# Optimization experiments

Measured on AMD Instinct MI355X. Metric: run time of the kernel, lower is better.

Reference implementation:

```python
import jax, jax.numpy as jnp
import numpy as np

N, D, K = 100000, 512, 1024

def setup_inputs() -> dict:
    key = jax.random.key(0)
    k1, k2 = jax.random.split(key)
    nodes = jax.random.normal(k1, (N, D), dtype=jnp.float32)
    # Faithful to original: indices sampled in [0, d) (torch.randint(d, ...))
    center_ind = jax.random.randint(k2, (K,), 0, D, dtype=jnp.int32)
    return {"nodes": nodes, "center_ind": center_ind, "num_clusters": K}


def reference(nodes, center_ind, num_clusters):
    # nodes: [n, d]; initial centers gathered from nodes (indices in [0, d) per original code)
    centers0 = nodes[center_ind]                      # [K, d]
    # Squared L2 distances via the expansion trick; avoids materializing [K, n, d].
    # argmin over squared distance == argmin over distance (sqrt is monotone).
    node_sq = jnp.sum(nodes * nodes, axis=1)          # [n]
    cent_sq = jnp.sum(centers0 * centers0, axis=1)    # [K]
    # d2[k, i] = ||c_k||^2 + ||x_i||^2 - 2 c_k . x_i
    d2 = cent_sq[:, None] + node_sq[None, :] - 2.0 * jnp.einsum("kd,nd->kn", centers0, nodes)
    assignment = jnp.argmin(d2, axis=0)               # [n]
    # Scatter-add nodes into their assigned cluster (index_add equivalent).
    centers = jax.ops.segment_sum(nodes, assignment, num_segments=num_clusters)  # [K, d]
    return centers
```

## Files before the change

### kernel.cpp

```cpp
#include <hip/hip_runtime.h>
#include <stdint.h>


typedef _Float16 f16x8  __attribute__((ext_vector_type(8)));
typedef float    f32x4  __attribute__((ext_vector_type(4)));

#define DD 512
#define KK 1024

static __device__ __forceinline__ unsigned orderable(float s) {
    unsigned u = __float_as_uint(s);
    return (u & 0x80000000u) ? ~u : (u | 0x80000000u);
}

__global__ void canon_first(const int* __restrict__ center_ind,
                            unsigned* __restrict__ firstk, int K) {
    int k = (int)(blockIdx.x * blockDim.x + threadIdx.x);
    if (k < K) atomicMin(&firstk[center_ind[k]], (unsigned)k);
}
__global__ void canon_map(const int* __restrict__ center_ind,
                          const unsigned* __restrict__ firstk,
                          unsigned* __restrict__ canon, int K) {
    int k = (int)(blockIdx.x * blockDim.x + threadIdx.x);
    if (k < K) canon[k] = firstk[center_ind[k]];
}

__global__ void gather_centers(const float* __restrict__ nodes,
                               const int* __restrict__ center_ind,
                               _Float16* __restrict__ centf,
                               float* __restrict__ cent_sq,
                               int K) {
    int k    = (int)blockIdx.x;
    int lane = (int)threadIdx.x;
    int ci   = center_ind[k];
    const f32x4* p = reinterpret_cast<const f32x4*>(nodes + (size_t)ci * DD + lane * 8);
    f32x4 v0 = p[0], v1 = p[1];
    f16x8 h;
    h[0]=(_Float16)v0[0]; h[1]=(_Float16)v0[1]; h[2]=(_Float16)v0[2]; h[3]=(_Float16)v0[3];
    h[4]=(_Float16)v1[0]; h[5]=(_Float16)v1[1]; h[6]=(_Float16)v1[2]; h[7]=(_Float16)v1[3];
    int t = k >> 4, r = k & 15;
    *reinterpret_cast<f16x8*>(centf + ((size_t)((t * 64 + lane) * 16 + r) << 3)) = h;
    float ssq = v0[0]*v0[0]+v0[1]*v0[1]+v0[2]*v0[2]+v0[3]*v0[3]
              + v1[0]*v1[0]+v1[1]*v1[1]+v1[2]*v1[2]+v1[3]*v1[3];
    #pragma unroll
    for (int off = 32; off > 0; off >>= 1) ssq += __shfl_xor(ssq, off, 64);
    if (lane == 0) cent_sq[k] = ssq;
}

__launch_bounds__(512, 4)
__global__ void assign_mfma(const float* __restrict__ nodes,
                            const _Float16* __restrict__ centf,
                            const float* __restrict__ cent_sq,
                            const unsigned* __restrict__ canon,
                            unsigned* __restrict__ assignment,
                            unsigned* __restrict__ counts,
                            int N, int K) {
    __shared__ __align__(16) _Float16 nt[64 * DD];
    __shared__ float csq[KK];
    __shared__ unsigned long long best[64];

    const int tid = (int)threadIdx.x;
    const int n0  = (int)blockIdx.x * 64;

    #pragma unroll
    for (int it = 0; it < 8; ++it) {
        int f   = it * 512 + tid;
        int row = f >> 6;
        int d0  = (f & 63) << 3;
        f32x4 v0 = {0.f,0.f,0.f,0.f}, v1 = {0.f,0.f,0.f,0.f};
        if (n0 + row < N) {
            const f32x4* p = reinterpret_cast<const f32x4*>(nodes + (size_t)(n0 + row) * DD + d0);
            v0 = p[0]; v1 = p[1];
        }
        f16x8 h;
        h[0]=(_Float16)v0[0]; h[1]=(_Float16)v0[1]; h[2]=(_Float16)v0[2]; h[3]=(_Float16)v0[3];
        h[4]=(_Float16)v1[0]; h[5]=(_Float16)v1[1]; h[6]=(_Float16)v1[2]; h[7]=(_Float16)v1[3];
        int byte = ((row << 10) + (d0 << 1)) ^ ((row & 7) << 4);
        *reinterpret_cast<f16x8*>(reinterpret_cast<char*>(nt) + byte) = h;
    }
    for (int j = tid; j < K;  j += 512) csq[j]  = cent_sq[j];
    for (int j = tid; j < 64; j += 512) best[j] = ~0ULL;
    __syncthreads();

    const int lane = tid & 63;
    const int wid  = tid >> 6;
    const int l15  = lane & 15;
    const int g    = lane >> 4;
    const int swz  = (l15 & 7) << 4;
    char* ntb = reinterpret_cast<char*>(nt);
    const int cw0 = wid * (K >> 3);

    int bbase[4];
    #pragma unroll
    for (int nG = 0; nG < 4; ++nG) bbase[nG] = (((nG * 16 + l15) << 10) + (g << 4));

    #define LA(dst, tg_, s_)                                                         \
        { _Pragma("unroll")                                                          \
          for (int t_ = 0; t_ < 2; ++t_)                                             \
              dst[t_] = *reinterpret_cast<const f16x8*>(                             \
                  centf + ((size_t)((cw0 >> 4) + (tg_) * 2 + t_) << 13)              \
                        + ((s_) << 9) + (lane << 3)); }
    #define LB(dst, s_)                                                              \
        { _Pragma("unroll")                                                          \
          for (int nG = 0; nG < 4; ++nG)                                             \
              dst[nG] = *reinterpret_cast<const f16x8*>(                             \
                  ntb + ((bbase[nG] + ((s_) << 6)) ^ swz)); }
    #define MM(Av, Bv)                                                               \
        { _Pragma("unroll")                                                          \
          for (int t_ = 0; t_ < 2; ++t_)                                             \
              _Pragma("unroll")                                                      \
              for (int nG = 0; nG < 4; ++nG)                                         \
                  acc[t_][nG] = __builtin_amdgcn_mfma_f32_16x16x32_f16(              \
                      Av[t_], Bv[nG], acc[t_][nG], 0, 0, 0); }

    f16x8 Av[2];
    f16x8 Bv[4];

    #pragma unroll
    for (int tg = 0; tg < 4; ++tg) {
        const int cbase = cw0 + tg * 32;

        f32x4 acc[2][4];
        #pragma unroll
        for (int a = 0; a < 2; ++a)
            #pragma unroll
            for (int b = 0; b < 4; ++b) { f32x4 z = {0.f,0.f,0.f,0.f}; acc[a][b] = z; }

        #pragma unroll
        for (int s = 0; s < 16; ++s) {
            LA(Av, tg, s);
            LB(Bv, s);
            MM(Av, Bv);
        }

        #pragma unroll
        for (int nG = 0; nG < 4; ++nG) {
            unsigned long long pk = ~0ULL;
            #pragma unroll
            for (int tC = 0; tC < 2; ++tC) {
                #pragma unroll
                for (int q = 0; q < 4; ++q) {
                    int c = cbase + tC * 16 + g * 4 + q;
                    float s = fmaf(-2.f, acc[tC][nG][q], csq[c]);
                    unsigned long long v =
                        ((unsigned long long)orderable(s) << 32) | (unsigned)c;
                    pk = v < pk ? v : pk;
                }
            }
            unsigned long long o;
            o = __shfl_xor(pk, 16, 64); pk = o < pk ? o : pk;
            o = __shfl_xor(pk, 32, 64); pk = o < pk ? o : pk;
            if (lane < 16) atomicMin(&best[nG * 16 + l15], pk);
        }
    }
    #undef LA
    #undef LB
    #undef MM

    __syncthreads();
    if (tid < 64 && n0 + tid < N) {
        unsigned k = (unsigned)(best[tid] & 0xffffffffu);
        k = canon[k];
        assignment[n0 + tid] = k;
        atomicAdd(&counts[k], 1u);
    }
}

__global__ void scan_offsets(const unsigned* __restrict__ counts,
                             unsigned* __restrict__ cursor) {
    __shared__ unsigned s[KK];
    int t = (int)threadIdx.x;
    unsigned c = counts[t];
    s[t] = c;
    __syncthreads();
    for (int off = 1; off < KK; off <<= 1) {
        unsigned v = (t >= off) ? s[t - off] : 0u;
        __syncthreads();
        s[t] += v;
        __syncthreads();
    }
    cursor[t] = s[t] - c;
}

__global__ void scatter_idx(const unsigned* __restrict__ assignment,
                            unsigned* __restrict__ cursor,
                            unsigned* __restrict__ keys, int N) {
    int i = (int)(blockIdx.x * blockDim.x + threadIdx.x);
    if (i < N) {
        unsigned k = assignment[i];
        unsigned slot = atomicAdd(&cursor[k], 1u);
        keys[slot] = (k << 20) | (unsigned)i;
    }
}

#define CHUNK 32
__launch_bounds__(256, 4)
__global__ void aggregate3(const float* __restrict__ nodes,
                           const unsigned* __restrict__ keys,
                           float* __restrict__ out, int N) {
    const int tid  = (int)threadIdx.x;
    const int wid  = tid >> 6;
    const int lane = tid & 63;
    const int base = ((int)blockIdx.x * 4 + wid) * CHUNK;
    if (base >= N) return;
    const int n    = min(CHUNK, N - base);

    int sI = base + (lane & 31);
    unsigned myk = (sI < N) ? keys[sI] : 0u;

    f32x4 a0 = {0.f,0.f,0.f,0.f}, a1 = {0.f,0.f,0.f,0.f};
    int curk = -1;
    auto flush = [&](void) {
        float* dst = out + ((size_t)curk << 9) + lane * 8;
        #pragma unroll
        for (int e = 0; e < 4; ++e) atomicAdd(dst + e, a0[e]);
        #pragma unroll
        for (int e = 0; e < 4; ++e) atomicAdd(dst + 4 + e, a1[e]);
    };

    int j = 0;
    while (j < n) {
        int b = n - j; if (b > 4) b = 4;
        f32x4 r[4][2];
        int   kk[4];
        #pragma unroll
        for (int t = 0; t < 4; ++t) {
            if (t < b) {
                unsigned key = __shfl(myk, j + t, 64);
                kk[t] = (int)(key >> 20);
                const f32x4* p = reinterpret_cast<const f32x4*>(
                    nodes + ((size_t)(key & 0xFFFFFu) << 9) + lane * 8);
                r[t][0] = p[0];
                r[t][1] = p[1];
            }
        }
        #pragma unroll
        for (int t = 0; t < 4; ++t) {
            if (t < b) {
                if (kk[t] != curk) {
                    if (curk >= 0) flush();
                    curk = kk[t];
                    f32x4 z = {0.f,0.f,0.f,0.f}; a0 = z; a1 = z;
                }
                a0 += r[t][0];
                a1 += r[t][1];
            }
        }
        j += 4;
    }
    if (curk >= 0) flush();
}

extern "C" void kernel_launch(void* const* d_in, const int* in_sizes, int n_in,
                              void* d_out, int out_size, void* d_ws, size_t ws_size,
                              hipStream_t stream) {
    const float* nodes      = (const float*)d_in[0];
    const int*   center_ind = (const int*)d_in[1];
    int K = in_sizes[1];
    int D = out_size / K;
    int N = in_sizes[0] / D;

    char* ws = (char*)d_ws;
    _Float16* centf      = (_Float16*)ws;
    size_t    o          = (size_t)K * DD * 2;
    float*    cent_sq    = (float*)(ws + o);    o += (size_t)K * 4;
    unsigned* assignment = (unsigned*)(ws + o); o += (size_t)N * 4;
    unsigned* counts     = (unsigned*)(ws + o); o += (size_t)K * 4;
    unsigned* cursor     = (unsigned*)(ws + o); o += (size_t)K * 4;
    unsigned* firstk     = (unsigned*)(ws + o); o += (size_t)D * 4;
    unsigned* canon      = (unsigned*)(ws + o); o += (size_t)K * 4;
    unsigned* keys       = (unsigned*)(ws + o); o += (size_t)N * 4;
    float*    out        = (float*)d_out;

    hipMemsetAsync(counts, 0, (size_t)K * sizeof(unsigned), stream);
    hipMemsetAsync(firstk, 0xFF, (size_t)D * sizeof(unsigned), stream);
    hipMemsetAsync(out, 0, (size_t)out_size * sizeof(float), stream);

    canon_first<<<(K + 255) / 256, 256, 0, stream>>>(center_ind, firstk, K);
    canon_map<<<(K + 255) / 256, 256, 0, stream>>>(center_ind, firstk, canon, K);
    gather_centers<<<K, 64, 0, stream>>>(nodes, center_ind, centf, cent_sq, K);
    assign_mfma<<<(N + 63) / 64, 512, 0, stream>>>(nodes, centf, cent_sq, canon,
                                                   assignment, counts, N, K);
    scan_offsets<<<1, KK, 0, stream>>>(counts, cursor);
    scatter_idx<<<(N + 255) / 256, 256, 0, stream>>>(assignment, cursor, keys, N);
    aggregate3<<<(N + 4 * CHUNK - 1) / (4 * CHUNK), 256, 0, stream>>>(nodes, keys, out, N);
}
```

Baseline: 525.7 us.

## Stage center tiles into LDS via async global_load_lds with double buffering

The assignment kernel drops from 512 to 256 threads. Center fragments are no longer read straight from global memory per wave; they are staged into a double-buffered LDS tile with global_load_lds, and all 4 waves share each 16-k slice. Argmin is now kept in registers across all center tiles, and the result goes to a global 64-bit atomicMin buffer, which a new finalize kernel reads to produce assignments and counts. This cuts redundant global and L2 traffic for the centers, but adds a __syncthreads per k-step, an extra kernel launch, and an N*8 memset.

```diff
diff --git a/kernel.cpp b/kernel.cpp
--- a/kernel.cpp
+++ b/kernel.cpp
@@ -11,6 +11,12 @@
 static __device__ __forceinline__ unsigned orderable(float s) {
     unsigned u = __float_as_uint(s);
     return (u & 0x80000000u) ? ~u : (u | 0x80000000u);
+}
+
+static __device__ __forceinline__ void gload_lds16(const void* gsrc, void* ldst) {
+    __builtin_amdgcn_global_load_lds(
+        (const __attribute__((address_space(1))) unsigned int*)gsrc,
+        (__attribute__((address_space(3))) unsigned int*)ldst, 16, 0, 0);
 }
 
 __global__ void canon_first(const int* __restrict__ center_ind,
@@ -47,24 +53,23 @@
     if (lane == 0) cent_sq[k] = ssq;
 }
 
-__launch_bounds__(512, 4)
+__launch_bounds__(256, 2)
 __global__ void assign_mfma(const float* __restrict__ nodes,
                             const _Float16* __restrict__ centf,
                             const float* __restrict__ cent_sq,
-                            const unsigned* __restrict__ canon,
-                            unsigned* __restrict__ assignment,
-                            unsigned* __restrict__ counts,
+                            unsigned long long* __restrict__ bestg,
                             int N, int K) {
     __shared__ __align__(16) _Float16 nt[64 * DD];
-    __shared__ float csq[KK];
-    __shared__ unsigned long long best[64];
+    __shared__ __align__(16) _Float16 ab[2][4096];
 
     const int tid = (int)threadIdx.x;
     const int n0  = (int)blockIdx.x * 64;
-
-    #pragma unroll
-    for (int it = 0; it < 8; ++it) {
-        int f   = it * 512 + tid;
+    const int lane = tid & 63;
+    const int wid  = tid >> 6;
+
+    #pragma unroll
+    for (int it = 0; it < 16; ++it) {
+        int f   = it * 256 + tid;
         int row = f >> 6;
         int d0  = (f & 63) << 3;
         f32x4 v0 = {0.f,0.f,0.f,0.f}, v1 = {0.f,0.f,0.f,0.f};
@@ -78,90 +83,104 @@
         int byte = ((row << 10) + (d0 << 1)) ^ ((row & 7) << 4);
         *reinterpret_cast<f16x8*>(reinterpret_cast<char*>(nt) + byte) = h;
     }
-    for (int j = tid; j < K;  j += 512) csq[j]  = cent_sq[j];
-    for (int j = tid; j < 64; j += 512) best[j] = ~0ULL;
-    __syncthreads();
-
-    const int lane = tid & 63;
-    const int wid  = tid >> 6;
-    const int l15  = lane & 15;
-    const int g    = lane >> 4;
-    const int swz  = (l15 & 7) << 4;
+
+    const int l15 = lane & 15;
+    const int g   = lane >> 4;
+    const int swz = (l15 & 7) << 4;
     char* ntb = reinterpret_cast<char*>(nt);
-    const int cw0 = wid * (K >> 3);
+    const char* cfb = reinterpret_cast<const char*>(centf);
 
     int bbase[4];
     #pragma unroll
     for (int nG = 0; nG < 4; ++nG) bbase[nG] = (((nG * 16 + l15) << 10) + (g << 4));
 
-    #define LA(dst, tg_, s_)                                                         \
-        { _Pragma("unroll")                                                          \
-          for (int t_ = 0; t_ < 2; ++t_)                                             \
-              dst[t_] = *reinterpret_cast<const f16x8*>(                             \
-                  centf + ((size_t)((cw0 >> 4) + (tg_) * 2 + t_) << 13)              \
-                        + ((s_) << 9) + (lane << 3)); }
-    #define LB(dst, s_)                                                              \
+    #define STAGE(buf_, gs_)                                                         \
+        { const int ct_ = (gs_) >> 4, s_ = (gs_) & 15;                               \
+          _Pragma("unroll")                                                          \
+          for (int i_ = 0; i_ < 2; ++i_) {                                           \
+              const int c_ = i_ * 4 + wid;                                           \
+              gload_lds16(cfb + (size_t)(ct_ * 8 + c_) * 16384                       \
+                              + (size_t)s_ * 1024 + lane * 16,                       \
+                          reinterpret_cast<char*>(&ab[buf_][0]) + c_ * 1024);        \
+          } }
+    #define LB(dst, s_)                                                             \
         { _Pragma("unroll")                                                          \
           for (int nG = 0; nG < 4; ++nG)                                             \
               dst[nG] = *reinterpret_cast<const f16x8*>(                             \
                   ntb + ((bbase[nG] + ((s_) << 6)) ^ swz)); }
-    #define MM(Av, Bv)                                                               \
-        { _Pragma("unroll")                                                          \
-          for (int t_ = 0; t_ < 2; ++t_)                                             \
-              _Pragma("unroll")                                                      \
-              for (int nG = 0; nG < 4; ++nG)                                         \
-                  acc[t_][nG] = __builtin_amdgcn_mfma_f32_16x16x32_f16(              \
-                      Av[t_], Bv[nG], acc[t_][nG], 0, 0, 0); }
-
-    f16x8 Av[2];
-    f16x8 Bv[4];
-
-    #pragma unroll
-    for (int tg = 0; tg < 4; ++tg) {
-        const int cbase = cw0 + tg * 32;
-
-        f32x4 acc[2][4];
+
+    f32x4 acc[2][4];
+    #pragma unroll
+    for (int a = 0; a < 2; ++a)
+        #pragma unroll
+        for (int b = 0; b < 4; ++b) { f32x4 z = {0.f,0.f,0.f,0.f}; acc[a][b] = z; }
+    unsigned long long pk[4] = {~0ULL, ~0ULL, ~0ULL, ~0ULL};
+
+    STAGE(0, 0);
+    __syncthreads();
+
+    for (int ct = 0; ct < 8; ++ct) {
+        #pragma unroll
+        for (int s = 0; s < 16; ++s) {
+            const int gs = ct * 16 + s;
+            if (gs + 1 < 128) STAGE((gs + 1) & 1, gs + 1);
+            const char* abb = reinterpret_cast<const char*>(&ab[gs & 1][0]);
+            f16x8 Afr[2], Bfr[4];
+            #pragma unroll
+            for (int t = 0; t < 2; ++t)
+                Afr[t] = *reinterpret_cast<const f16x8*>(
+                    abb + ((2 * wid + t) << 10) + (lane << 4));
+            LB(Bfr, s);
+            #pragma unroll
+            for (int t = 0; t < 2; ++t)
+                #pragma unroll
+                for (int nG = 0; nG < 4; ++nG)
+                    acc[t][nG] = __builtin_amdgcn_mfma_f32_16x16x32_f16(
+                        Afr[t], Bfr[nG], acc[t][nG], 0, 0, 0);
+            __syncthreads();
+        }
+
+        #pragma unroll
+        for (int tC = 0; tC < 2; ++tC) {
+            const int cb = ct * 128 + wid * 32 + tC * 16 + g * 4;
+            f32x4 cs = *reinterpret_cast<const f32x4*>(cent_sq + cb);
+            #pragma unroll
+            for (int nG = 0; nG < 4; ++nG) {
+                #pragma unroll
+                for (int q = 0; q < 4; ++q) {
+                    float sc = fmaf(-2.f, acc[tC][nG][q], cs[q]);
+                    unsigned long long v =
+                        ((unsigned long long)orderable(sc) << 32) | (unsigned)(cb + q);
+                    pk[nG] = v < pk[nG] ? v : pk[nG];
+                }
+            }
+        }
         #pragma unroll
         for (int a = 0; a < 2; ++a)
             #pragma unroll
             for (int b = 0; b < 4; ++b) { f32x4 z = {0.f,0.f,0.f,0.f}; acc[a][b] = z; }
-
-        #pragma unroll
-        for (int s = 0; s < 16; ++s) {
-            LA(Av, tg, s);
-            LB(Bv, s);
-            MM(Av, Bv);
-        }
-
-        #pragma unroll
-        for (int nG = 0; nG < 4; ++nG) {
-            unsigned long long pk = ~0ULL;
-            #pragma unroll
-            for (int tC = 0; tC < 2; ++tC) {
-                #pragma unroll
-                for (int q = 0; q < 4; ++q) {
-                    int c = cbase + tC * 16 + g * 4 + q;
-                    float s = fmaf(-2.f, acc[tC][nG][q], csq[c]);
-                    unsigned long long v =
-                        ((unsigned long long)orderable(s) << 32) | (unsigned)c;
-                    pk = v < pk ? v : pk;
-                }
-            }
-            unsigned long long o;
-            o = __shfl_xor(pk, 16, 64); pk = o < pk ? o : pk;
-            o = __shfl_xor(pk, 32, 64); pk = o < pk ? o : pk;
-            if (lane < 16) atomicMin(&best[nG * 16 + l15], pk);
-        }
-    }
-    #undef LA
+    }
+    #undef STAGE
     #undef LB
-    #undef MM
-
-    __syncthreads();
-    if (tid < 64 && n0 + tid < N) {
-        unsigned k = (unsigned)(best[tid] & 0xffffffffu);
-        k = canon[k];
-        assignment[n0 + tid] = k;
+
+    #pragma unroll
+    for (int nG = 0; nG < 4; ++nG) {
+        unsigned long long p = pk[nG], o;
+        o = __shfl_xor(p, 16, 64); p = o < p ? o : p;
+        o = __shfl_xor(p, 32, 64); p = o < p ? o : p;
+        int n = n0 + nG * 16 + l15;
+        if (lane < 16 && n < N) atomicMin(&bestg[n], p);
+    }
+}
+
+__global__ void finalize(const unsigned long long* __restrict__ bestg,
+                         const unsigned* __restrict__ canon,
+                         unsigned* __restrict__ assignment,
+                         unsigned* __restrict__ counts, int N) {
+    int i = (int)(blockIdx.x * blockDim.x + threadIdx.x);
+    if (i < N) {
+        unsigned k = canon[(unsigned)(bestg[i] & 0xffffffffu)];
+        assignment[i] = k;
         atomicAdd(&counts[k], 1u);
     }
 }
@@ -270,17 +289,20 @@
     unsigned* firstk     = (unsigned*)(ws + o); o += (size_t)D * 4;
     unsigned* canon      = (unsigned*)(ws + o); o += (size_t)K * 4;
     unsigned* keys       = (unsigned*)(ws + o); o += (size_t)N * 4;
+    o = (o + 7) & ~(size_t)7;
+    unsigned long long* bestg = (unsigned long long*)(ws + o); o += (size_t)N * 8;
     float*    out        = (float*)d_out;
 
     hipMemsetAsync(counts, 0, (size_t)K * sizeof(unsigned), stream);
     hipMemsetAsync(firstk, 0xFF, (size_t)D * sizeof(unsigned), stream);
+    hipMemsetAsync(bestg, 0xFF, (size_t)N * sizeof(unsigned long long), stream);
     hipMemsetAsync(out, 0, (size_t)out_size * sizeof(float), stream);
 
     canon_first<<<(K + 255) / 256, 256, 0, stream>>>(center_ind, firstk, K);
     canon_map<<<(K + 255) / 256, 256, 0, stream>>>(center_ind, firstk, canon, K);
     gather_centers<<<K, 64, 0, stream>>>(nodes, center_ind, centf, cent_sq, K);
-    assign_mfma<<<(N + 63) / 64, 512, 0, stream>>>(nodes, centf, cent_sq, canon,
-                                                   assignment, counts, N, K);
+    assign_mfma<<<(N + 63) / 64, 256, 0, stream>>>(nodes, centf, cent_sq, bestg, N, K);
+    finalize<<<(N + 255) / 256, 256, 0, stream>>>(bestg, canon, assignment, counts, N);
     scan_offsets<<<1, KK, 0, stream>>>(counts, cursor);
     scatter_idx<<<(N + 255) / 256, 256, 0, stream>>>(assignment, cursor, keys, N);
     aggregate3<<<(N + 4 * CHUNK - 1) / (4 * CHUNK), 256, 0, stream>>>(nodes, keys, out, N);
```

Result: slower. 579.0 us (+10.1%).
